# Kernel optimization log

Hardware: AMD Instinct MI355X
Metric: run time of the kernel (lower is better)

## Reference

```python
import jax, jax.numpy as jnp
import numpy as np

N, E, IN_DIM, HID, G = 100000, 3200000, 128, 64, 256


def setup_inputs() -> dict:
    key = jax.random.key(0)
    ks = jax.random.split(key, 10)
    x = jax.random.normal(ks[0], (N, IN_DIM), dtype=jnp.float32)
    ei = jax.random.randint(ks[1], (2, E), 0, N, dtype=jnp.int64)
    ew = jax.random.uniform(ks[2], (E,), dtype=jnp.float32)
    batch = jnp.sort(jax.random.randint(ks[3], (N,), 0, G, dtype=jnp.int64))
    W1 = jax.random.normal(ks[4], (IN_DIM, HID), dtype=jnp.float32) * 0.05
    b1 = jnp.zeros((HID,), dtype=jnp.float32)
    W2 = jax.random.normal(ks[5], (HID, HID), dtype=jnp.float32) * 0.05
    b2 = jnp.zeros((HID,), dtype=jnp.float32)
    Wc = jax.random.normal(ks[6], (HID, 1), dtype=jnp.float32) * 0.05
    bc = jnp.zeros((1,), dtype=jnp.float32)
    return {"x": x, "ei": ei, "ew": ew, "batch": batch,
            "W1": W1, "b1": b1, "W2": W2, "b2": b2, "Wc": Wc, "bc": bc}


def _gcn_norm(ei, ew, n):
    # PyG gcn_norm: add self-loops (weight 1), symmetric deg^-1/2 normalization
    loop = jnp.arange(n, dtype=ei.dtype)
    row = jnp.concatenate([ei[0], loop])
    col = jnp.concatenate([ei[1], loop])
    w = jnp.concatenate([ew, jnp.ones((n,), dtype=ew.dtype)])
    deg = jax.ops.segment_sum(w, col, num_segments=n)
    dis = jnp.where(deg > 0, jax.lax.rsqrt(jnp.maximum(deg, 1e-30)), 0.0)
    norm = dis[row] * w * dis[col]
    return row, col, norm


def _gcn_conv(x, row, col, norm, W, b, n):
    xl = x @ W                                   # [N, hid]
    msg = xl[row] * norm[:, None]                # gather + scale, [E+N, hid]
    return jax.ops.segment_sum(msg, col, num_segments=n) + b


def reference(x, ei, ew, batch, W1, b1, W2, b2, Wc, bc):
    n = x.shape[0]
    row, col, norm = _gcn_norm(ei, ew, n)
    h = jax.nn.relu(_gcn_conv(x, row, col, norm, W1, b1, n))
    h = jax.nn.relu(_gcn_conv(h, row, col, norm, W2, b2, n))
    # global mean pool over graphs
    sums = jax.ops.segment_sum(h, batch, num_segments=G)           # [G, hid]
    cnt = jax.ops.segment_sum(jnp.ones((n,), h.dtype), batch, num_segments=G)
    pooled = sums / jnp.maximum(cnt, 1.0)[:, None]
    return (pooled @ Wc + bc).reshape(-1)                           # [G]
```

## Files before the change

### kernel.cpp

```cpp
#include <hip/hip_runtime.h>

#define N_NODES 100000
#define N_PAD   100352
#define N_EDGES 3200000
#define IN_DIM  128
#define HID     64
#define N_GRAPHS 256
#define NB      392
#define NBLK    256
#define EPB     (N_EDGES / NBLK)
#define G1ROWS  64
#define G1BLK   (N_PAD / G1ROWS)

typedef unsigned short ushort_t;
typedef unsigned int   uint_t;
typedef __attribute__((ext_vector_type(4))) float f32x4;
typedef __attribute__((ext_vector_type(8))) short bf16x8;

__device__ __forceinline__ ushort_t f2bf(float v) {
    uint_t b = __float_as_uint(v);
    b += 0x7fffu + ((b >> 16) & 1u);
    return (ushort_t)(b >> 16);
}
__device__ __forceinline__ void bf2f2(uint_t u, float& lo, float& hi) {
    lo = __uint_as_float(u << 16);
    hi = __uint_as_float(u & 0xffff0000u);
}
__device__ __forceinline__ void ld_bf16x8(const ushort_t* p, float4& a, float4& b) {
    uint4 u = *(const uint4*)p;
    bf2f2(u.x, a.x, a.y); bf2f2(u.y, a.z, a.w);
    bf2f2(u.z, b.x, b.y); bf2f2(u.w, b.z, b.w);
}
__device__ __forceinline__ void fma8(float4& a0, float4& a1, const uint4& u, float w) {
    float lo, hi;
    bf2f2(u.x, lo, hi); a0.x += lo * w; a0.y += hi * w;
    bf2f2(u.y, lo, hi); a0.z += lo * w; a0.w += hi * w;
    bf2f2(u.z, lo, hi); a1.x += lo * w; a1.y += hi * w;
    bf2f2(u.w, lo, hi); a1.z += lo * w; a1.w += hi * w;
}
__device__ __forceinline__ int2 ldrec(const int2* __restrict__ csr, int last, int idx) {
    int2 r = csr[idx <= last ? idx : last];
    if (idx > last) r.y = 0;
    return r;
}

__global__ __launch_bounds__(256) void wtprep_kernel(const float* __restrict__ W1,
                                                     ushort_t* __restrict__ Wt) {
    int i = blockIdx.x * 256 + threadIdx.x;
    int k = i >> 6, c = i & 63;
    float w = W1[i];
    ushort_t hi = f2bf(w);
    float rem = w - __uint_as_float((uint_t)hi << 16);
    ushort_t lo = f2bf(rem);
    Wt[c * 128 + k]        = hi;
    Wt[8192 + c * 128 + k] = lo;
}

__global__ __launch_bounds__(256) void bhist_gemm1_kernel(
        const int* __restrict__ col, int* __restrict__ H,
        const float* __restrict__ x, const ushort_t* __restrict__ Wt,
        ushort_t* __restrict__ xl) {
    __shared__ char smem[49152];
    int tid = threadIdx.x;
    if (blockIdx.x < NBLK) {
        int (*h)[NB] = (int (*)[NB])smem;
        for (int i = tid; i < NB; i += 256) { h[0][i] = 0; h[1][i] = 0; }
        __syncthreads();
        const int4* col4 = (const int4*)col;
        int base4 = blockIdx.x * (EPB / 4);
        int sel = tid & 1;
        for (int j = tid; j < EPB / 4; j += 256) {
            int4 c = col4[base4 + j];
            atomicAdd(&h[sel][c.x >> 8], 1);
            atomicAdd(&h[sel][c.y >> 8], 1);
            atomicAdd(&h[sel][c.z >> 8], 1);
            atomicAdd(&h[sel][c.w >> 8], 1);
        }
        __syncthreads();
        for (int i = tid; i < NB; i += 256) H[i * NBLK + blockIdx.x] = h[0][i] + h[1][i];
    } else {
        int bid = blockIdx.x - NBLK;
        ushort_t* sA  = (ushort_t*)smem;
        ushort_t* sBh = sA + 8192;
        ushort_t* sBl = sBh + 8192;
        int r0 = bid * G1ROWS;
        {
            int row = tid >> 2;
            int ck  = (tid & 3) * 32;
            int gr  = r0 + row; if (gr >= N_NODES) gr = 0;
            const float4* xs = (const float4*)(x + (size_t)gr * IN_DIM + ck);
            #pragma unroll
            for (int j = 0; j < 4; ++j) {
                float4 a = xs[2 * j], b = xs[2 * j + 1];
                uint4 u;
                u.x = (uint_t)f2bf(a.x) | ((uint_t)f2bf(a.y) << 16);
                u.y = (uint_t)f2bf(a.z) | ((uint_t)f2bf(a.w) << 16);
                u.z = (uint_t)f2bf(b.x) | ((uint_t)f2bf(b.y) << 16);
                u.w = (uint_t)f2bf(b.z) | ((uint_t)f2bf(b.w) << 16);
                int byte = (row * 256 + ck * 2 + j * 16) ^ ((row & 7) << 4);
                *(uint4*)(smem + byte) = u;
            }
            const uint4* wh = (const uint4*)Wt;
            const uint4* wl = (const uint4*)(Wt + 8192);
            #pragma unroll
            for (int j = 0; j < 4; ++j) {
                int u16  = tid * 4 + j;
                int colb = u16 >> 4, kc = u16 & 15;
                int byte = (colb * 256 + kc * 16) ^ ((colb & 7) << 4);
                *(uint4*)((char*)sBh + byte) = wh[u16];
                *(uint4*)((char*)sBl + byte) = wl[u16];
            }
        }
        __syncthreads();
        int wv   = tid >> 6, lane = tid & 63;
        int m0   = wv * 16;
        int fr   = lane & 15;
        int fkb  = (lane >> 4) * 16;
        int arow = m0 + fr;
        int aswz = (arow & 7) << 4;
        int bswz = (fr & 7) << 4;
        f32x4 acc0 = {0.f, 0.f, 0.f, 0.f}, acc1 = acc0, acc2 = acc0, acc3 = acc0;
        #pragma unroll
        for (int ks = 0; ks < 4; ++ks) {
            int kb = ks * 64 + fkb;
            bf16x8 af = *(const bf16x8*)((const char*)sA + ((arow * 256 + kb) ^ aswz));
#define BSTEP(ACC, n0) { \
            int bb = (((n0 + fr) * 256 + kb) ^ bswz); \
            bf16x8 bh = *(const bf16x8*)((const char*)sBh + bb); \
            bf16x8 bl = *(const bf16x8*)((const char*)sBl + bb); \
            ACC = __builtin_amdgcn_mfma_f32_16x16x32_bf16(af, bh, ACC, 0, 0, 0); \
            ACC = __builtin_amdgcn_mfma_f32_16x16x32_bf16(af, bl, ACC, 0, 0, 0); }
            BSTEP(acc0, 0) BSTEP(acc1, 16) BSTEP(acc2, 32) BSTEP(acc3, 48)
#undef BSTEP
        }
        __syncthreads();
        ushort_t* sO = (ushort_t*)smem;
        int orow = m0 + (lane >> 4) * 4;
#define TSTORE(reg) { ushort_t* sp = sO + (orow + reg) * 72; \
        sp[fr]      = f2bf(acc0[reg]); sp[fr + 16] = f2bf(acc1[reg]); \
        sp[fr + 32] = f2bf(acc2[reg]); sp[fr + 48] = f2bf(acc3[reg]); }
        TSTORE(0) TSTORE(1) TSTORE(2) TSTORE(3)
#undef TSTORE
        __syncthreads();
        int r  = tid >> 2;
        int cb = (tid & 3) * 16;
        int gr2 = r0 + r;
        if (gr2 < N_NODES) {
            const uint4* sp = (const uint4*)(sO + r * 72 + cb);
            uint4* dp = (uint4*)(xl + (size_t)gr2 * HID + cb);
            dp[0] = sp[0];
            dp[1] = sp[1];
        }
    }
}

__global__ __launch_bounds__(256) void scan1_kernel(int* H, int* __restrict__ bsum) {
    __shared__ int s[256];
    int i = blockIdx.x * 256 + threadIdx.x;
    int v = H[i];
    s[threadIdx.x] = v;
    __syncthreads();
    #pragma unroll
    for (int off = 1; off < 256; off <<= 1) {
        int t = (threadIdx.x >= off) ? s[threadIdx.x - off] : 0;
        __syncthreads();
        s[threadIdx.x] += t;
        __syncthreads();
    }
    H[i] = s[threadIdx.x] - v;
    if (threadIdx.x == 255) bsum[blockIdx.x] = s[255];
}

__global__ __launch_bounds__(256) void bscatter_kernel(const int* __restrict__ row,
                                                       const int* __restrict__ col,
                                                       const float* __restrict__ ew,
                                                       const int* __restrict__ H,
                                                       const int* __restrict__ bsum,
                                                       int* __restrict__ boff,
                                                       int2* __restrict__ recs) {
    __shared__ int2 lrec[EPB];
    __shared__ int  lofs[NB];
    __shared__ int  hcnt[NB];
    __shared__ int  gofs[NB];
    __shared__ int  cur[NB];
    __shared__ int  s[256];
    __shared__ int  carry;
    int tid = threadIdx.x, blk = blockIdx.x;
    if (tid == 0) carry = 0;
    __syncthreads();
    for (int c = 0; c < 2; ++c) {
        int i = c * 256 + tid;
        int v = (i < NB) ? bsum[i] : 0;
        s[tid] = v;
        __syncthreads();
        #pragma unroll
        for (int off = 1; off < 256; off <<= 1) {
            int t = (tid >= off) ? s[tid - off] : 0;
            __syncthreads();
            s[tid] += t;
            __syncthreads();
        }
        if (i < NB) {
            int tb = s[tid] - v + carry;
            int ex = H[i * NBLK + blk];
            gofs[i] = tb + ex;
            hcnt[i] = ((blk < NBLK - 1) ? H[i * NBLK + blk + 1] : v) - ex;
            if (blk == 0) boff[i] = tb;
        }
        __syncthreads();
        if (tid == 0) carry += s[255];
        __syncthreads();
    }
    if (tid == 0) carry = 0;
    __syncthreads();
    for (int c = 0; c < 2; ++c) {
        int i = c * 256 + tid;
        int v = (i < NB) ? hcnt[i] : 0;
        s[tid] = v;
        __syncthreads();
        #pragma unroll
        for (int off = 1; off < 256; off <<= 1) {
            int t = (tid >= off) ? s[tid - off] : 0;
            __syncthreads();
            s[tid] += t;
            __syncthreads();
        }
        if (i < NB) { int l = s[tid] - v + carry; lofs[i] = l; cur[i] = l; }
        __syncthreads();
        if (tid == 0) carry += s[255];
        __syncthreads();
    }
    const int4*   row4 = (const int4*)row;
    const int4*   col4 = (const int4*)col;
    const float4* ew4  = (const float4*)ew;
    int base4 = blk * (EPB / 4);
    for (int j = tid; j < EPB / 4; j += 256) {
        int4   r4 = row4[base4 + j];
        int4   c4 = col4[base4 + j];
        float4 w4 = ew4[base4 + j];
        int p0 = atomicAdd(&cur[c4.x >> 8], 1);
        lrec[p0] = make_int2(r4.x | ((c4.x & 255) << 17), __float_as_int(w4.x));
        int p1 = atomicAdd(&cur[c4.y >> 8], 1);
        lrec[p1] = make_int2(r4.y | ((c4.y & 255) << 17), __float_as_int(w4.y));
        int p2 = atomicAdd(&cur[c4.z >> 8], 1);
        lrec[p2] = make_int2(r4.z | ((c4.z & 255) << 17), __float_as_int(w4.z));
        int p3 = atomicAdd(&cur[c4.w >> 8], 1);
        lrec[p3] = make_int2(r4.w | ((c4.w & 255) << 17), __float_as_int(w4.w));
    }
    __syncthreads();
    int wv = tid >> 6, lane = tid & 63;
    for (int i = wv; i < NB; i += 4) {
        int cnt = hcnt[i], lo = lofs[i], go = gofs[i];
        for (int k = lane; k < cnt; k += 64)
            recs[go + k] = lrec[lo + k];
    }
}

__global__ __launch_bounds__(1024) void degcsr_kernel(const int2* __restrict__ recs,
                                                      const int* __restrict__ boff,
                                                      float* __restrict__ dis,
                                                      int* __restrict__ rowptr,
                                                      int2* __restrict__ csr,
                                                      ushort_t* xl) {
    __shared__ int   cnt[256];
    __shared__ float degf[256];
    __shared__ int   sscan[256];
    __shared__ int   cur[256];
    int b = blockIdx.x, tid = threadIdx.x;
    if (tid < 256) { cnt[tid] = 0; degf[tid] = 0.f; }
    __syncthreads();
    int s = boff[b], e = (b + 1 < NB) ? boff[b + 1] : N_EDGES;
    for (int j = s + tid; j < e; j += 1024) {
        int2 r = recs[j];
        int cl = (r.x >> 17) & 255;
        atomicAdd(&cnt[cl], 1);
        atomicAdd(&degf[cl], __int_as_float(r.y));
    }
    __syncthreads();
    int c = (tid < 256) ? cnt[tid] : 0;
    if (tid < 256) sscan[tid] = c;
    __syncthreads();
    #pragma unroll
    for (int off = 1; off < 256; off <<= 1) {
        int t = (tid < 256 && tid >= off) ? sscan[tid - off] : 0;
        __syncthreads();
        if (tid < 256) sscan[tid] += t;
        __syncthreads();
    }
    float d = 0.f;
    if (tid < 256) {
        int rp = s + sscan[tid] - c;
        rowptr[b * 256 + tid] = rp;
        cur[tid] = rp;
        d = 1.0f / sqrtf(fmaxf(1.0f + degf[tid], 1e-30f));
        dis[b * 256 + tid] = d;
    }
    __syncthreads();
    if (tid < 256) degf[tid] = d;
    __syncthreads();
    for (int j = s + tid; j < e; j += 1024) {
        int2 r = recs[j];
        int cl = (r.x >> 17) & 255;
        int pos = atomicAdd(&cur[cl], 1);
        csr[pos] = r;
    }
    int n0 = b * 256;
    for (int i = tid; i < 256 * 8; i += 1024) {
        int r = i >> 3;
        int n = n0 + r;
        if (n >= N_NODES) break;
        uint4* p = (uint4*)(xl + (size_t)n * HID) + (i & 7);
        float d2 = degf[r];
        uint4 u = *p;
        float lo, hi;
        uint_t w0, w1, w2, w3;
        bf2f2(u.x, lo, hi); w0 = f2bf(lo * d2) | ((uint_t)f2bf(hi * d2) << 16);
        bf2f2(u.y, lo, hi); w1 = f2bf(lo * d2) | ((uint_t)f2bf(hi * d2) << 16);
        bf2f2(u.z, lo, hi); w2 = f2bf(lo * d2) | ((uint_t)f2bf(hi * d2) << 16);
        bf2f2(u.w, lo, hi); w3 = f2bf(lo * d2) | ((uint_t)f2bf(hi * d2) << 16);
        *p = make_uint4(w0, w1, w2, w3);
    }
}

__device__ __forceinline__ void gather_row16(const int2* __restrict__ csr,
                                             const ushort_t* __restrict__ xl,
                                             int base, int end, int n,
                                             int g, int c0, int lane,
                                             float4& a0, float4& a1) {
    a0 = make_float4(0.f, 0.f, 0.f, 0.f);
    a1 = make_float4(0.f, 0.f, 0.f, 0.f);
    if (g == 0) {
        ld_bf16x8(xl + (uint_t)(n * HID + c0), a0, a1);
    }
    int tot  = end - base;
    int half = (tot + 1) >> 1;
    int gs   = base + (g ? half : 0);
    int m    = g ? (tot - half) : half;
    if (m > 0) {
        int last = gs + m - 1;
        int li4  = lane & 3;
        int gb   = lane & 56;
        int nb   = (m + 3) >> 2;

#define BCI(r_, u0_, u1_, u2_, u3_, w0_, w1_, w2_, w3_) do {                     \
        int r0_ = __shfl((r_).x, gb + 0, 64), r1_ = __shfl((r_).x, gb + 1, 64);  \
        int r2_ = __shfl((r_).x, gb + 2, 64), r3_ = __shfl((r_).x, gb + 3, 64);  \
        w0_ = __int_as_float(__shfl((r_).y, gb + 0, 64));                         \
        w1_ = __int_as_float(__shfl((r_).y, gb + 1, 64));                         \
        w2_ = __int_as_float(__shfl((r_).y, gb + 2, 64));                         \
        w3_ = __int_as_float(__shfl((r_).y, gb + 3, 64));                         \
        u0_ = *(const uint4*)(xl + (uint_t)((r0_ & 0x1FFFF) * HID + c0));         \
        u1_ = *(const uint4*)(xl + (uint_t)((r1_ & 0x1FFFF) * HID + c0));         \
        u2_ = *(const uint4*)(xl + (uint_t)((r2_ & 0x1FFFF) * HID + c0));         \
        u3_ = *(const uint4*)(xl + (uint_t)((r3_ & 0x1FFFF) * HID + c0));         \
    } while (0)

        uint4 uA0, uA1, uA2, uA3, uB0, uB1, uB2, uB3;
        float wA0, wA1, wA2, wA3, wB0, wB1, wB2, wB3;
        int2 rA = ldrec(csr, last, gs + li4);
        int2 rB = (nb > 1) ? ldrec(csr, last, gs + 4 + li4) : rA;
        BCI(rA, uA0, uA1, uA2, uA3, wA0, wA1, wA2, wA3);
        int blk = 0;
        while (true) {
            bool hasB  = (blk + 1 < nb);
            bool hasA2 = (blk + 2 < nb);
            if (hasA2) rA = ldrec(csr, last, gs + (blk + 2) * 4 + li4);
            if (hasB) { BCI(rB, uB0, uB1, uB2, uB3, wB0, wB1, wB2, wB3); }
            fma8(a0, a1, uA0, wA0); fma8(a0, a1, uA1, wA1);
            fma8(a0, a1, uA2, wA2); fma8(a0, a1, uA3, wA3);
            if (!hasB) break;
            bool hasB2 = (blk + 3 < nb);
            if (hasB2) rB = ldrec(csr, last, gs + (blk + 3) * 4 + li4);
            if (hasA2) { BCI(rA, uA0, uA1, uA2, uA3, wA0, wA1, wA2, wA3); }
            fma8(a0, a1, uB0, wB0); fma8(a0, a1, uB1, wB1);
            fma8(a0, a1, uB2, wB2); fma8(a0, a1, uB3, wB3);
            if (!hasA2) break;
            blk += 2;
        }
#undef BCI
    }
    a0.x += __shfl_down(a0.x, 8, 64); a0.y += __shfl_down(a0.y, 8, 64);
    a0.z += __shfl_down(a0.z, 8, 64); a0.w += __shfl_down(a0.w, 8, 64);
    a1.x += __shfl_down(a1.x, 8, 64); a1.y += __shfl_down(a1.y, 8, 64);
    a1.z += __shfl_down(a1.z, 8, 64); a1.w += __shfl_down(a1.w, 8, 64);
}

__global__ __launch_bounds__(256) void gather_gemm2_kernel(
        const int2* __restrict__ csr, const int* __restrict__ rowptr,
        const float* __restrict__ dis, const ushort_t* __restrict__ xl,
        const float* __restrict__ W2, const float* __restrict__ b1,
        ushort_t* __restrict__ xl2) {
    __shared__ float sW[HID * HID];
    __shared__ float sh[16][HID + 4];
    int tid = threadIdx.x;
    const float4* W4  = (const float4*)W2;
    float4*       sW4 = (float4*)sW;
    #pragma unroll
    for (int i = 0; i < 4; ++i) sW4[tid + 256 * i] = W4[tid + 256 * i];

    int n0   = blockIdx.x * 16;
    int wv   = tid >> 6;
    int lane = tid & 63;
    int lr   = wv * 4 + (lane >> 4);
    int n    = n0 + lr;
    int g    = (lane >> 3) & 1;
    int c0   = (lane & 7) << 3;
    int base = rowptr[n], end = rowptr[n + 1];
    float d  = dis[n];
    float4 a0, a1;
    gather_row16(csr, xl, base, end, n, g, c0, lane, a0, a1);
    if (g == 0) {
        float4 bb0 = *(const float4*)(b1 + c0);
        float4 bb1 = *(const float4*)(b1 + c0 + 4);
        float4 h0 = make_float4(fmaxf(a0.x * d + bb0.x, 0.f), fmaxf(a0.y * d + bb0.y, 0.f),
                                fmaxf(a0.z * d + bb0.z, 0.f), fmaxf(a0.w * d + bb0.w, 0.f));
        float4 h1 = make_float4(fmaxf(a1.x * d + bb1.x, 0.f), fmaxf(a1.y * d + bb1.y, 0.f),
                                fmaxf(a1.z * d + bb1.z, 0.f), fmaxf(a1.w * d + bb1.w, 0.f));
        *(float4*)(&sh[lr][c0])     = h0;
        *(float4*)(&sh[lr][c0 + 4]) = h1;
    }
    __syncthreads();
    int cc = tid & 63, rq = tid >> 6;
    float acc0 = 0.f, acc1 = 0.f, acc2 = 0.f, acc3 = 0.f;
    #pragma unroll 8
    for (int k = 0; k < HID; ++k) {
        float wk = sW[k * HID + cc];
        acc0 += sh[rq * 4 + 0][k] * wk;
        acc1 += sh[rq * 4 + 1][k] * wk;
        acc2 += sh[rq * 4 + 2][k] * wk;
        acc3 += sh[rq * 4 + 3][k] * wk;
    }
    xl2[(size_t)(n0 + rq * 4 + 0) * HID + cc] = f2bf(acc0 * dis[n0 + rq * 4 + 0]);
    xl2[(size_t)(n0 + rq * 4 + 1) * HID + cc] = f2bf(acc1 * dis[n0 + rq * 4 + 1]);
    xl2[(size_t)(n0 + rq * 4 + 2) * HID + cc] = f2bf(acc2 * dis[n0 + rq * 4 + 2]);
    xl2[(size_t)(n0 + rq * 4 + 3) * HID + cc] = f2bf(acc3 * dis[n0 + rq * 4 + 3]);
}

__global__ __launch_bounds__(256) void gather_pool_kernel(
        const int2* __restrict__ csr, const int* __restrict__ rowptr,
        const float* __restrict__ dis, const ushort_t* __restrict__ xl,
        const float* __restrict__ b2, const float* __restrict__ Wc,
        float* __restrict__ sval) {
    int tid  = threadIdx.x;
    int n    = (blockIdx.x * 256 + tid) >> 4;
    int lane = tid & 63;
    int g    = (lane >> 3) & 1;
    int c0   = (lane & 7) << 3;
    int base = rowptr[n], end = rowptr[n + 1];
    float d  = dis[n];
    float4 a0, a1;
    gather_row16(csr, xl, base, end, n, g, c0, lane, a0, a1);
    float4 bb0 = *(const float4*)(b2 + c0);
    float4 bb1 = *(const float4*)(b2 + c0 + 4);
    float4 wc0 = *(const float4*)(Wc + c0);
    float4 wc1 = *(const float4*)(Wc + c0 + 4);
    float s = fmaxf(a0.x * d + bb0.x, 0.f) * wc0.x + fmaxf(a0.y * d + bb0.y, 0.f) * wc0.y
            + fmaxf(a0.z * d + bb0.z, 0.f) * wc0.z + fmaxf(a0.w * d + bb0.w, 0.f) * wc0.w
            + fmaxf(a1.x * d + bb1.x, 0.f) * wc1.x + fmaxf(a1.y * d + bb1.y, 0.f) * wc1.y
            + fmaxf(a1.z * d + bb1.z, 0.f) * wc1.z + fmaxf(a1.w * d + bb1.w, 0.f) * wc1.w;
    s += __shfl_down(s, 4, 64);
    s += __shfl_down(s, 2, 64);
    s += __shfl_down(s, 1, 64);
    if ((lane & 15) == 0) sval[n] = s;
}

__global__ __launch_bounds__(256) void final_out_kernel(const float* __restrict__ sval,
                                                        const int* __restrict__ batch,
                                                        const float* __restrict__ bc,
                                                        float* __restrict__ out) {
    __shared__ float s[256];
    int g = blockIdx.x;
    int lo = 0, hi = N_NODES;
    while (lo < hi) { int m = (lo + hi) >> 1; if (batch[m] < g) lo = m + 1; else hi = m; }
    int start = lo;
    hi = N_NODES;
    while (lo < hi) { int m = (lo + hi) >> 1; if (batch[m] < g + 1) lo = m + 1; else hi = m; }
    int end = lo;
    float acc = 0.f;
    for (int i = start + threadIdx.x; i < end; i += 256) acc += sval[i];
    s[threadIdx.x] = acc;
    __syncthreads();
    #pragma unroll
    for (int off = 128; off > 0; off >>= 1) {
        if (threadIdx.x < off) s[threadIdx.x] += s[threadIdx.x + off];
        __syncthreads();
    }
    if (threadIdx.x == 0)
        out[g] = s[0] / fmaxf((float)(end - start), 1.0f) + bc[0];
}

extern "C" void kernel_launch(void* const* d_in, const int* in_sizes, int n_in,
                              void* d_out, int out_size, void* d_ws, size_t ws_size,
                              hipStream_t stream) {
    const float* x     = (const float*)d_in[0];
    const int*   ei    = (const int*)  d_in[1];
    const float* ew    = (const float*)d_in[2];
    const int*   batch = (const int*)  d_in[3];
    const float* W1    = (const float*)d_in[4];
    const float* b1    = (const float*)d_in[5];
    const float* W2    = (const float*)d_in[6];
    const float* b2    = (const float*)d_in[7];
    const float* Wc    = (const float*)d_in[8];
    const float* bc    = (const float*)d_in[9];
    float* out = (float*)d_out;

    const int* row = ei;
    const int* col = ei + N_EDGES;

    int2*     recs   = (int2*)d_ws;
    ushort_t* xlA    = (ushort_t*)(recs + N_EDGES);
    ushort_t* xlB    = xlA + (size_t)N_NODES * HID;
    int2*     csr    = (int2*)(xlB + (size_t)N_NODES * HID);
    int*      rowptr = (int*)(csr + N_EDGES);
    float*    dis    = (float*)(rowptr + N_PAD);
    int*      bsum   = (int*)(dis + N_PAD);
    int*      boff   = bsum + 512;
    float*    sval   = (float*)(boff + 512);
    int*      H      = (int*)csr;
    ushort_t* Wt     = (ushort_t*)recs;

    wtprep_kernel   <<<32,   256, 0, stream>>>(W1, Wt);
    bhist_gemm1_kernel<<<NBLK + G1BLK, 256, 0, stream>>>(col, H, x, Wt, xlA);
    scan1_kernel    <<<NB,   256, 0, stream>>>(H, bsum);
    bscatter_kernel <<<NBLK, 256, 0, stream>>>(row, col, ew, H, bsum, boff, recs);
    degcsr_kernel   <<<NB,  1024, 0, stream>>>(recs, boff, dis, rowptr, csr, xlA);
    gather_gemm2_kernel<<<N_NODES / 16, 256, 0, stream>>>(csr, rowptr, dis, xlA, W2, b1, xlB);
    gather_pool_kernel <<<N_NODES / 16, 256, 0, stream>>>(csr, rowptr, dis, xlB, b2, Wc, sval);
    final_out_kernel<<<N_GRAPHS, 256, 0, stream>>>(sval, batch, bc, out);
}
```

Measured before the change: 339.1 us.

## Reorder nodes by in-degree to balance gather work across wavefronts

Builds a degree histogram inside degcsr_kernel, scans it in descending-degree order, and scatters node ids into a permutation array. The two gather kernels then process nodes in that order, so the 16-lane groups of a wavefront handle rows of similar length. The aim is to cut idle lanes caused by uneven neighbour counts. In exchange it adds two small kernels plus an indirection, and writes to xl2 and reads of rowptr and dis become scattered instead of contiguous.

New measurement: 364.3 us. 7.4% more time.

```diff
diff --git a/kernel.cpp b/kernel.cpp
--- a/kernel.cpp
+++ b/kernel.cpp
@@ -11,6 +11,7 @@
 #define EPB     (N_EDGES / NBLK)
 #define G1ROWS  64
 #define G1BLK   (N_PAD / G1ROWS)
+#define DBINS   1024
 
 typedef unsigned short ushort_t;
 typedef unsigned int   uint_t;
@@ -45,8 +46,10 @@
 }
 
 __global__ __launch_bounds__(256) void wtprep_kernel(const float* __restrict__ W1,
-                                                     ushort_t* __restrict__ Wt) {
+                                                     ushort_t* __restrict__ Wt,
+                                                     int* __restrict__ hist) {
     int i = blockIdx.x * 256 + threadIdx.x;
+    if (i < DBINS) hist[i] = 0;
     int k = i >> 6, c = i & 63;
     float w = W1[i];
     ushort_t hi = f2bf(w);
@@ -261,13 +264,16 @@
                                                       float* __restrict__ dis,
                                                       int* __restrict__ rowptr,
                                                       int2* __restrict__ csr,
-                                                      ushort_t* xl) {
+                                                      ushort_t* xl,
+                                                      int* __restrict__ hist) {
     __shared__ int   cnt[256];
     __shared__ float degf[256];
     __shared__ int   sscan[256];
     __shared__ int   cur[256];
+    __shared__ int   lh[DBINS];
     int b = blockIdx.x, tid = threadIdx.x;
     if (tid < 256) { cnt[tid] = 0; degf[tid] = 0.f; }
+    lh[tid] = 0;
     __syncthreads();
     int s = boff[b], e = (b + 1 < NB) ? boff[b + 1] : N_EDGES;
     for (int j = s + tid; j < e; j += 1024) {
@@ -278,8 +284,13 @@
     }
     __syncthreads();
     int c = (tid < 256) ? cnt[tid] : 0;
-    if (tid < 256) sscan[tid] = c;
-    __syncthreads();
+    if (tid < 256) {
+        sscan[tid] = c;
+        int node = b * 256 + tid;
+        if (node < N_NODES) atomicAdd(&lh[c > (DBINS - 1) ? (DBINS - 1) : c], 1);
+    }
+    __syncthreads();
+    if (lh[tid] > 0) atomicAdd(&hist[tid], lh[tid]);
     #pragma unroll
     for (int off = 1; off < 256; off <<= 1) {
         int t = (tid < 256 && tid >= off) ? sscan[tid - off] : 0;
@@ -320,6 +331,50 @@
         bf2f2(u.w, lo, hi); w3 = f2bf(lo * d2) | ((uint_t)f2bf(hi * d2) << 16);
         *p = make_uint4(w0, w1, w2, w3);
     }
+}
+
+__global__ __launch_bounds__(1024) void permscan_kernel(const int* __restrict__ hist,
+                                                        int* __restrict__ binofs) {
+    __shared__ int s[DBINS];
+    int t = threadIdx.x;
+    int orig = hist[DBINS - 1 - t];
+    s[t] = orig;
+    __syncthreads();
+    for (int off = 1; off < DBINS; off <<= 1) {
+        int v = (t >= off) ? s[t - off] : 0;
+        __syncthreads();
+        s[t] += v;
+        __syncthreads();
+    }
+    binofs[DBINS - 1 - t] = s[t] - orig;
+}
+
+__global__ __launch_bounds__(256) void permscat_kernel(const int* __restrict__ rowptr,
+                                                       int* __restrict__ binofs,
+                                                       int* __restrict__ nperm) {
+    __shared__ int lh[DBINS];
+    __shared__ int lbase[DBINS];
+    int tid = threadIdx.x;
+    #pragma unroll
+    for (int j = 0; j < 4; ++j) lh[tid * 4 + j] = 0;
+    __syncthreads();
+    int n = blockIdx.x * 256 + tid;
+    int deg = 0, lpos = 0;
+    bool valid = (n < N_NODES);
+    if (valid) {
+        deg = rowptr[n + 1] - rowptr[n];
+        if (deg > DBINS - 1) deg = DBINS - 1;
+        lpos = atomicAdd(&lh[deg], 1);
+    }
+    __syncthreads();
+    #pragma unroll
+    for (int j = 0; j < 4; ++j) {
+        int bin = tid * 4 + j;
+        int cc = lh[bin];
+        if (cc > 0) lbase[bin] = atomicAdd(&binofs[bin], cc);
+    }
+    __syncthreads();
+    if (valid) nperm[lbase[deg] + lpos] = n;
 }
 
 __device__ __forceinline__ void gather_row16(const int2* __restrict__ csr,
@@ -389,22 +444,23 @@
         const int2* __restrict__ csr, const int* __restrict__ rowptr,
         const float* __restrict__ dis, const ushort_t* __restrict__ xl,
         const float* __restrict__ W2, const float* __restrict__ b1,
-        ushort_t* __restrict__ xl2) {
+        const int* __restrict__ nperm, ushort_t* __restrict__ xl2) {
     __shared__ float sW[HID * HID];
     __shared__ float sh[16][HID + 4];
+    __shared__ int   nid[16];
     int tid = threadIdx.x;
     const float4* W4  = (const float4*)W2;
     float4*       sW4 = (float4*)sW;
     #pragma unroll
     for (int i = 0; i < 4; ++i) sW4[tid + 256 * i] = W4[tid + 256 * i];
 
-    int n0   = blockIdx.x * 16;
     int wv   = tid >> 6;
     int lane = tid & 63;
     int lr   = wv * 4 + (lane >> 4);
-    int n    = n0 + lr;
+    int n    = nperm[blockIdx.x * 16 + lr];
     int g    = (lane >> 3) & 1;
     int c0   = (lane & 7) << 3;
+    if ((lane & 15) == 0) nid[lr] = n;
     int base = rowptr[n], end = rowptr[n + 1];
     float d  = dis[n];
     float4 a0, a1;
@@ -430,19 +486,21 @@
         acc2 += sh[rq * 4 + 2][k] * wk;
         acc3 += sh[rq * 4 + 3][k] * wk;
     }
-    xl2[(size_t)(n0 + rq * 4 + 0) * HID + cc] = f2bf(acc0 * dis[n0 + rq * 4 + 0]);
-    xl2[(size_t)(n0 + rq * 4 + 1) * HID + cc] = f2bf(acc1 * dis[n0 + rq * 4 + 1]);
-    xl2[(size_t)(n0 + rq * 4 + 2) * HID + cc] = f2bf(acc2 * dis[n0 + rq * 4 + 2]);
-    xl2[(size_t)(n0 + rq * 4 + 3) * HID + cc] = f2bf(acc3 * dis[n0 + rq * 4 + 3]);
+    int o0 = nid[rq * 4 + 0], o1 = nid[rq * 4 + 1];
+    int o2 = nid[rq * 4 + 2], o3 = nid[rq * 4 + 3];
+    xl2[(size_t)o0 * HID + cc] = f2bf(acc0 * dis[o0]);
+    xl2[(size_t)o1 * HID + cc] = f2bf(acc1 * dis[o1]);
+    xl2[(size_t)o2 * HID + cc] = f2bf(acc2 * dis[o2]);
+    xl2[(size_t)o3 * HID + cc] = f2bf(acc3 * dis[o3]);
 }
 
 __global__ __launch_bounds__(256) void gather_pool_kernel(
         const int2* __restrict__ csr, const int* __restrict__ rowptr,
         const float* __restrict__ dis, const ushort_t* __restrict__ xl,
         const float* __restrict__ b2, const float* __restrict__ Wc,
-        float* __restrict__ sval) {
+        const int* __restrict__ nperm, float* __restrict__ sval) {
     int tid  = threadIdx.x;
-    int n    = (blockIdx.x * 256 + tid) >> 4;
+    int n    = nperm[(blockIdx.x * 256 + tid) >> 4];
     int lane = tid & 63;
     int g    = (lane >> 3) & 1;
     int c0   = (lane & 7) << 3;
@@ -518,13 +576,18 @@
     float*    sval   = (float*)(boff + 512);
     int*      H      = (int*)csr;
     ushort_t* Wt     = (ushort_t*)recs;
-
-    wtprep_kernel   <<<32,   256, 0, stream>>>(W1, Wt);
+    int*      nperm  = (int*)recs + 32768;
+    int*      hist   = (int*)xlB;
+    int*      binofs = hist + DBINS;
+
+    wtprep_kernel   <<<32,   256, 0, stream>>>(W1, Wt, hist);
     bhist_gemm1_kernel<<<NBLK + G1BLK, 256, 0, stream>>>(col, H, x, Wt, xlA);
     scan1_kernel    <<<NB,   256, 0, stream>>>(H, bsum);
     bscatter_kernel <<<NBLK, 256, 0, stream>>>(row, col, ew, H, bsum, boff, recs);
-    degcsr_kernel   <<<NB,  1024, 0, stream>>>(recs, boff, dis, rowptr, csr, xlA);
-    gather_gemm2_kernel<<<N_NODES / 16, 256, 0, stream>>>(csr, rowptr, dis, xlA, W2, b1, xlB);
-    gather_pool_kernel <<<N_NODES / 16, 256, 0, stream>>>(csr, rowptr, dis, xlB, b2, Wc, sval);
+    degcsr_kernel   <<<NB,  1024, 0, stream>>>(recs, boff, dis, rowptr, csr, xlA, hist);
+    permscan_kernel <<<1,   1024, 0, stream>>>(hist, binofs);
+    permscat_kernel <<<NB,   256, 0, stream>>>(rowptr, binofs, nperm);
+    gather_gemm2_kernel<<<N_NODES / 16, 256, 0, stream>>>(csr, rowptr, dis, xlA, W2, b1, nperm, xlB);
+    gather_pool_kernel <<<N_NODES / 16, 256, 0, stream>>>(csr, rowptr, dis, xlB, b2, Wc, nperm, sval);
     final_out_kernel<<<N_GRAPHS, 256, 0, stream>>>(sval, batch, bc, out);
 }
```
